# Optimization experiments

Measured on AMD Instinct MI355X. Metric: run time of the kernel, lower is better.

The kernel has to match this reference:

```python
import jax, jax.numpy as jnp
import numpy as np

L, D, H, HD, M = 4096, 1024, 16, 64, 4096
EPS = 1e-5


def setup_inputs() -> dict:
    key = jax.random.key(0)
    ks = jax.random.split(key, 12)
    hidden_states = jax.random.normal(ks[0], (L, D), dtype=jnp.float32)
    cu_seqlens = jnp.arange(5, dtype=jnp.int32) * (L // 4)  # [0,1024,2048,3072,4096]
    # rope freqs as cos/sin of random angles: (L, HD//2, 2)
    angles = jax.random.uniform(ks[1], (L, HD // 2), dtype=jnp.float32) * (2.0 * np.pi)
    rope_freqs = jnp.stack([jnp.cos(angles), jnp.sin(angles)], axis=-1)
    s = 0.02
    params = {
        "ln0_g": jnp.ones((D,), jnp.float32), "ln0_b": jnp.zeros((D,), jnp.float32),
        "ln1_g": jnp.ones((D,), jnp.float32), "ln1_b": jnp.zeros((D,), jnp.float32),
        "w_qkv": jax.random.normal(ks[2], (D, 3 * D), jnp.float32) * s,
        "w_o":   jax.random.normal(ks[3], (D, D), jnp.float32) * s,
        "w_fc0": jax.random.normal(ks[4], (D, M), jnp.float32) * s,
        "b_fc0": jnp.zeros((M,), jnp.float32),
        "w_fc1": jax.random.normal(ks[5], (M, D), jnp.float32) * s,
        "b_fc1": jnp.zeros((D,), jnp.float32),
    }
    return {"hidden_states": hidden_states, "cu_seqlens": cu_seqlens, "rope_freqs": rope_freqs, **params}


def _layernorm(x, g, b):
    mu = jnp.mean(x, axis=-1, keepdims=True)
    var = jnp.var(x, axis=-1, keepdims=True)
    return (x - mu) * jax.lax.rsqrt(var + EPS) * g + b


def _apply_rope(x, fc):
    # x: (L, H, HD); fc: (L, HD//2, 2) -> broadcast over heads
    xr = x.reshape(L, H, HD // 2, 2)
    a, b = xr[..., 0], xr[..., 1]
    c, s = fc[:, None, :, 0], fc[:, None, :, 1]
    out = jnp.stack([a * c - b * s, a * s + b * c], axis=-1)
    return out.reshape(L, H, HD)


def reference(hidden_states, cu_seqlens, rope_freqs, ln0_g, ln0_b, ln1_g, ln1_b,
              w_qkv, w_o, w_fc0, b_fc0, w_fc1, b_fc1):
    residual = hidden_states
    x = _layernorm(hidden_states, ln0_g, ln0_b)
    qkv = (x @ w_qkv).reshape(L, 3, H, HD)
    q, k, v = qkv[:, 0], qkv[:, 1], qkv[:, 2]
    q = _apply_rope(q, rope_freqs)
    k = _apply_rope(k, rope_freqs)
    # block-diagonal mask from cu_seqlens
    seg = jnp.searchsorted(cu_seqlens[1:], jnp.arange(L, dtype=cu_seqlens.dtype), side="right")
    mask = seg[:, None] == seg[None, :]  # (L, L)
    scale = 1.0 / np.sqrt(HD)
    scores = jnp.einsum("lhd,mhd->hlm", q, k) * scale
    scores = jnp.where(mask[None], scores, jnp.float32(-1e30))
    probs = jax.nn.softmax(scores, axis=-1)
    attn = jnp.einsum("hlm,mhd->lhd", probs, v).reshape(L, D)
    attn = attn @ w_o
    h = residual + attn
    y = _layernorm(h, ln1_g, ln1_b)
    y = jax.nn.gelu(y @ w_fc0 + b_fc0, approximate=False) @ w_fc1 + b_fc1
    return h + y
```

## Files before the change

### kernel.cpp

```cpp
#include <hip/hip_runtime.h>
#include <cstdint>
#include <cmath>

#define L_ 4096
#define D_ 1024
#define H_ 16
#define HD_ 64
#define M_ 4096

typedef __bf16 bf16_t;
typedef __attribute__((ext_vector_type(8))) __bf16 bf16x8;
typedef __attribute__((ext_vector_type(4))) __bf16 bf16x4;
typedef __attribute__((ext_vector_type(4))) float f32x4;

#define WAIT_VM0 0x0f70
#define WAIT_LGKM0 0xc07f

__device__ __forceinline__ f32x4 mfma16(bf16x8 a, bf16x8 b, f32x4 c) {
    return __builtin_amdgcn_mfma_f32_16x16x32_bf16(a, b, c, 0, 0, 0);
}

__device__ __forceinline__ void gload_lds16(const bf16_t* g, bf16_t* l) {
    __builtin_amdgcn_global_load_lds(
        (const __attribute__((address_space(1))) unsigned int*)(g),
        (__attribute__((address_space(3))) unsigned int*)(l), 16, 0, 0);
}

__device__ __forceinline__ float fast_exp2(float x) {
    float r;
    asm volatile("v_exp_f32 %0, %1" : "=v"(r) : "v"(x));
    return r;
}
__device__ __forceinline__ float fast_rcp(float x) {
    float r;
    asm volatile("v_rcp_f32 %0, %1" : "=v"(r) : "v"(x));
    return r;
}
__device__ __forceinline__ float gelu_f(float v) {
    float t = v * (0.7978845608f + 0.0356774081f * v * v);
    return v * fast_rcp(1.f + fast_exp2(-2.885390082f * t));
}

__global__ __launch_bounds__(256) void ln_kernel(const float* __restrict__ x,
                                                 const float* __restrict__ g,
                                                 const float* __restrict__ b,
                                                 bf16_t* __restrict__ out) {
    int row = blockIdx.x, tid = threadIdx.x;
    int wave = tid >> 6, lane = tid & 63;
    const f32x4* xr = (const f32x4*)(x + (long)row * D_);
    f32x4 v = xr[tid];
    float s = v.x + v.y + v.z + v.w;
    __shared__ float red[8];
#pragma unroll
    for (int off = 32; off > 0; off >>= 1) s += __shfl_down(s, off, 64);
    if (lane == 0) red[wave] = s;
    __syncthreads();
    float mean = (red[0] + red[1] + red[2] + red[3]) * (1.f / 1024.f);
    float s2 = 0.f;
#pragma unroll
    for (int i = 0; i < 4; i++) { float d = v[i] - mean; s2 += d * d; }
#pragma unroll
    for (int off = 32; off > 0; off >>= 1) s2 += __shfl_down(s2, off, 64);
    __syncthreads();
    if (lane == 0) red[wave] = s2;
    __syncthreads();
    float var = (red[0] + red[1] + red[2] + red[3]) * (1.f / 1024.f);
    float rstd = rsqrtf(var + 1e-5f);
    f32x4 g4 = ((const f32x4*)g)[tid];
    f32x4 b4 = ((const f32x4*)b)[tid];
    bf16x4 o;
#pragma unroll
    for (int i = 0; i < 4; i++) o[i] = (bf16_t)((v[i] - mean) * rstd * g4[i] + b4[i]);
    *(bf16x4*)(out + (long)row * D_ + tid * 4) = o;
}

__global__ __launch_bounds__(256) void transpose_all(
    const float* __restrict__ w_qkv, const float* __restrict__ w_o,
    const float* __restrict__ w_fc0, const float* __restrict__ w_fc1,
    bf16_t* __restrict__ t_qkv, bf16_t* __restrict__ t_o,
    bf16_t* __restrict__ t_fc0, bf16_t* __restrict__ t_fc1) {
    __shared__ float t[32][33];
    int bidx = blockIdx.x;
    const float* W;
    bf16_t* Wt;
    int K, N, tile;
    if (bidx < 3072) { W = w_qkv; Wt = t_qkv; K = 1024; N = 3072; tile = bidx; }
    else if (bidx < 4096) { W = w_o; Wt = t_o; K = 1024; N = 1024; tile = bidx - 3072; }
    else if (bidx < 8192) { W = w_fc0; Wt = t_fc0; K = 1024; N = 4096; tile = bidx - 4096; }
    else { W = w_fc1; Wt = t_fc1; K = 4096; N = 1024; tile = bidx - 8192; }
    int nt = N >> 5;
    int n0 = (tile % nt) * 32, k0 = (tile / nt) * 32;
    int tx = threadIdx.x & 31, ty = threadIdx.x >> 5;
#pragma unroll
    for (int r = 0; r < 32; r += 8)
        t[ty + r][tx] = W[(long)(k0 + ty + r) * N + n0 + tx];
    __syncthreads();
#pragma unroll
    for (int r = 0; r < 32; r += 8)
        Wt[(long)(n0 + ty + r) * K + k0 + tx] = (bf16_t)t[tx][ty + r];
}

__global__ __launch_bounds__(256) void vt_kernel(const bf16_t* __restrict__ qkv,
                                                 bf16_t* __restrict__ Vt) {
    __shared__ bf16_t t[32][33];
    int l0 = blockIdx.x * 32, c0 = blockIdx.y * 32;
    int tx = threadIdx.x & 31, ty = threadIdx.x >> 5;
#pragma unroll
    for (int r = 0; r < 32; r += 8)
        t[ty + r][tx] = qkv[(long)(l0 + ty + r) * 3072 + 2048 + c0 + tx];
    __syncthreads();
#pragma unroll
    for (int r = 0; r < 32; r += 8)
        Vt[(long)(c0 + ty + r) * 4096 + l0 + tx] = t[tx][ty + r];
}

__global__ __launch_bounds__(256) void rope_kernel(bf16_t* __restrict__ qkv,
                                                   const float* __restrict__ freqs) {
    const float k1 = 0.125f * 1.44269504089f;
    int idx = blockIdx.x * 256 + threadIdx.x;
    int g = idx & 7;
    int h = (idx >> 3) & 15;
    int l = idx >> 7;
    const float* f = freqs + (long)l * 64 + g * 8;
    f32x4 f0 = ((const f32x4*)f)[0];
    f32x4 f1 = ((const f32x4*)f)[1];
    float c[4] = {f0.x, f0.z, f1.x, f1.z};
    float s[4] = {f0.y, f0.w, f1.y, f1.w};
    bf16_t* qp = qkv + (long)l * 3072 + h * 64 + g * 8;
    bf16x8 q = *(bf16x8*)qp;
    bf16x8 k = *(bf16x8*)(qp + 1024);
    bf16x8 qo, ko;
#pragma unroll
    for (int e = 0; e < 4; e++) {
        float a = (float)q[2 * e], b = (float)q[2 * e + 1];
        qo[2 * e] = (bf16_t)((a * c[e] - b * s[e]) * k1);
        qo[2 * e + 1] = (bf16_t)((a * s[e] + b * c[e]) * k1);
        a = (float)k[2 * e]; b = (float)k[2 * e + 1];
        ko[2 * e] = (bf16_t)(a * c[e] - b * s[e]);
        ko[2 * e + 1] = (bf16_t)(a * s[e] + b * c[e]);
    }
    *(bf16x8*)qp = qo;
    *(bf16x8*)(qp + 1024) = ko;
}

#define STAGE_A(d, h, kt)                                                          \
    gload_lds16(aSt + (long)((h) * 128) * K + (kt), &SA[d][h][(wv * 16) * 64]);    \
    gload_lds16(aSt + (long)((h) * 128 + 8) * K + (kt), &SA[d][h][(wv * 16 + 8) * 64]);

#define STAGE_B(d, h, kt)                                                          \
    gload_lds16(bSt + (long)((h) * 128) * K + (kt), &SB[d][h][(wv * 16) * 64]);    \
    gload_lds16(bSt + (long)((h) * 128 + 8) * K + (kt), &SB[d][h][(wv * 16 + 8) * 64]);

#define RD_A(dst, src, rq)                                                          \
    _Pragma("unroll") for (int i_ = 0; i_ < 4; i_++) {                              \
        dst[i_][0] = *(const bf16x8*)&src[((rq) * 64 + i_ * 16 + l16) * 64 + sl0 * 8]; \
        dst[i_][1] = *(const bf16x8*)&src[((rq) * 64 + i_ * 16 + l16) * 64 + sl1 * 8]; \
    }

#define RD_B(dst, src, cq)                                                          \
    _Pragma("unroll") for (int j_ = 0; j_ < 2; j_++) {                              \
        dst[j_][0] = *(const bf16x8*)&src[(bro + (cq) * 32 + j_ * 16 + l16) * 64 + sl0 * 8]; \
        dst[j_][1] = *(const bf16x8*)&src[(bro + (cq) * 32 + j_ * 16 + l16) * 64 + sl1 * 8]; \
    }

#define MFMA_Q(rq, cq, Af, Bf)                                                      \
    _Pragma("unroll") for (int i_ = 0; i_ < 4; i_++)                                \
    _Pragma("unroll") for (int j_ = 0; j_ < 2; j_++) {                              \
        acc[(rq) * 4 + i_][(cq) * 2 + j_] =                                         \
            mfma16(Af[i_][0], Bf[j_][0], acc[(rq) * 4 + i_][(cq) * 2 + j_]);        \
        acc[(rq) * 4 + i_][(cq) * 2 + j_] =                                         \
            mfma16(Af[i_][1], Bf[j_][1], acc[(rq) * 4 + i_][(cq) * 2 + j_]);        \
    }

#define LGKM0() asm volatile("s_waitcnt lgkmcnt(0)" ::: "memory")
#define VMC(n) asm volatile("s_waitcnt vmcnt(" #n ")" ::: "memory")
#define BAR() __builtin_amdgcn_s_barrier()
#define PRIO1() __builtin_amdgcn_s_setprio(1)
#define PRIO0() __builtin_amdgcn_s_setprio(0)

template <int EPI>
__device__ __forceinline__ void gemm256_core(
    const bf16_t* __restrict__ A, const bf16_t* __restrict__ Bt,
    int K, int N, long bm, long bn, int kb, int ke,
    bf16_t* __restrict__ outB, const float* __restrict__ bias) {
    __shared__ __align__(16) bf16_t SA[2][2][128 * 64];
    __shared__ __align__(16) bf16_t SB[2][2][128 * 64];
    int tid = threadIdx.x;
    int wv = tid >> 6, lane = tid & 63;
    int quad = lane >> 4, l16 = lane & 15;
    int wm = wv >> 2, wn = wv & 3;
    int lr = lane >> 3;
    int sc = (lane & 7) ^ (lr & 7);
    int sl0 = quad ^ (l16 & 7);
    int sl1 = (4 + quad) ^ (l16 & 7);
    int bro = (wn & 1) * 64;

    const bf16_t* aSt = A + (bm + wv * 16 + lr) * (long)K + sc * 8;
    const bf16_t* bSt = Bt + (bn + wv * 16 + lr) * (long)K + sc * 8;
    const bf16_t* pa0 = SA[0][wm];
    const bf16_t* pa1 = SA[1][wm];
    const bf16_t* pb0 = SB[0][wn >> 1];
    const bf16_t* pb1 = SB[1][wn >> 1];

    f32x4 acc[8][4];
#pragma unroll
    for (int i = 0; i < 8; i++)
#pragma unroll
        for (int j = 0; j < 4; j++) acc[i][j] = (f32x4){0.f, 0.f, 0.f, 0.f};

    bf16x8 a0[4][2], a1[4][2], b0[2][2], b1[2][2];

    STAGE_B(0, 0, kb); STAGE_A(0, 0, kb); STAGE_B(0, 1, kb); STAGE_A(0, 1, kb);
    STAGE_B(1, 0, kb + 64); STAGE_A(1, 0, kb + 64); STAGE_B(1, 1, kb + 64);
    VMC(6);
    BAR();
    RD_A(a0, pa0, 0); RD_B(b0, pb0, 0);
    LGKM0();

    for (int k0 = kb; k0 < ke; k0 += 128) {
        int kt2 = (k0 + 128 < ke) ? k0 + 128 : kb;
        int kt3 = kt2 + 64;
        BAR(); STAGE_A(1, 1, k0 + 64);
        PRIO1(); MFMA_Q(0, 0, a0, b0); PRIO0();
        RD_B(b1, pb0, 1); LGKM0();
        BAR(); STAGE_B(0, 0, kt2);
        PRIO1(); MFMA_Q(0, 1, a0, b1); PRIO0();
        RD_A(a1, pa0, 1); LGKM0();
        BAR(); STAGE_A(0, 0, kt2);
        PRIO1(); MFMA_Q(1, 0, a1, b0); PRIO0();
        VMC(4);
        BAR(); STAGE_B(0, 1, kt2);
        PRIO1(); MFMA_Q(1, 1, a1, b1); PRIO0();
        RD_A(a0, pa1, 0); RD_B(b0, pb1, 0); LGKM0();
        BAR(); STAGE_A(0, 1, kt2);
        PRIO1(); MFMA_Q(0, 0, a0, b0); PRIO0();
        RD_B(b1, pb1, 1); LGKM0();
        BAR(); STAGE_B(1, 0, kt3);
        PRIO1(); MFMA_Q(0, 1, a0, b1); PRIO0();
        RD_A(a1, pa1, 1); LGKM0();
        BAR(); STAGE_A(1, 0, kt3);
        PRIO1(); MFMA_Q(1, 0, a1, b0); PRIO0();
        VMC(4);
        BAR(); STAGE_B(1, 1, kt3);
        PRIO1(); MFMA_Q(1, 1, a1, b1); PRIO0();
        RD_A(a0, pa0, 0); RD_B(b0, pb0, 0); LGKM0();
    }
    VMC(0);

#pragma unroll
    for (int ri = 0; ri < 8; ri++)
#pragma unroll
        for (int cj = 0; cj < 4; cj++)
#pragma unroll
            for (int r = 0; r < 4; r++) {
                long row = bm + wm * 128 + (ri >> 2) * 64 + (ri & 3) * 16 + quad * 4 + r;
                long col = bn + wn * 64 + (cj >> 1) * 32 + (cj & 1) * 16 + l16;
                long idx = row * (long)N + col;
                float v = acc[ri][cj][r];
                if (EPI == 0) {
                    outB[idx] = (bf16_t)v;
                } else {
                    v += bias[col];
                    outB[idx] = (bf16_t)gelu_f(v);
                }
            }
}

__global__ __launch_bounds__(512) void gemm256_qkv(const bf16_t* __restrict__ A,
                                                   const bf16_t* __restrict__ Bt,
                                                   bf16_t* __restrict__ outB) {
    int g = blockIdx.x & 7, w = blockIdx.x >> 3;
    int gm = g >> 2, gn = g & 3;
    long bm = (long)(gm * 8 + w / 3) * 256;
    long bn = (long)(gn * 3 + w % 3) * 256;
    gemm256_core<0>(A, Bt, 1024, 3072, bm, bn, 0, 1024, outB, nullptr);
}

__global__ __launch_bounds__(512) void gemm256_fc0(const bf16_t* __restrict__ A,
                                                   const bf16_t* __restrict__ Bt,
                                                   bf16_t* __restrict__ outB,
                                                   const float* __restrict__ bias) {
    int g = blockIdx.x & 7, w = blockIdx.x >> 3;
    int gm = g >> 2, gn = g & 3;
    long bm = (long)(gm * 8 + (w >> 2)) * 256;
    long bn = (long)(gn * 4 + (w & 3)) * 256;
    gemm256_core<2>(A, Bt, 1024, 4096, bm, bn, 0, 1024, outB, bias);
}

__global__ __launch_bounds__(512) void gemm256_fc1(const bf16_t* __restrict__ A,
                                                   const bf16_t* __restrict__ Bt,
                                                   bf16_t* __restrict__ P) {
    int g = blockIdx.x & 7, w = blockIdx.x >> 3;
    int z = g >> 1, gm = g & 1;
    long bm = (long)(gm * 8 + (w >> 2)) * 256;
    long bn = (long)(w & 3) * 256;
    gemm256_core<0>(A, Bt, 4096, 1024, bm, bn, z * 1024, z * 1024 + 1024,
                    P + (long)z * L_ * D_, nullptr);
}

__global__ __launch_bounds__(256) void reduce_fc1(const bf16_t* __restrict__ P,
                                                  const float* __restrict__ bias,
                                                  float* __restrict__ out) {
    long i = (long)blockIdx.x * 256 + threadIdx.x;
    f32x4 b = ((const f32x4*)bias)[i & 255];
    f32x4 v = ((f32x4*)out)[i];
#pragma unroll
    for (int z = 0; z < 4; z++) {
        bf16x4 p = ((const bf16x4*)(P + (long)z * L_ * D_))[i];
#pragma unroll
        for (int e = 0; e < 4; e++) v[e] += (float)p[e];
    }
    v.x += b.x; v.y += b.y; v.z += b.z; v.w += b.w;
    ((f32x4*)out)[i] = v;
}

__global__ __launch_bounds__(256) void gemm_bt64_res(const bf16_t* __restrict__ A,
                                                     const bf16_t* __restrict__ Bt,
                                                     int M, int N, int K,
                                                     float* __restrict__ outF,
                                                     const float* __restrict__ res) {
    __shared__ __align__(16) bf16_t As[128 * 64];
    __shared__ __align__(16) bf16_t Bs[64 * 64];
    int tid = threadIdx.x;
    int wave = tid >> 6, lane = tid & 63;
    int quad = lane >> 4, l16 = lane & 15;

    int g = blockIdx.x & 7, w = blockIdx.x >> 3;
    int bn_i = w & 15, bm_i = g * 4 + (w >> 4);
    long bm = (long)bm_i * 128, bn = (long)bn_i * 64;

    f32x4 acc[2][4];
#pragma unroll
    for (int i = 0; i < 2; i++)
#pragma unroll
        for (int j = 0; j < 4; j++) acc[i][j] = (f32x4){0.f, 0.f, 0.f, 0.f};

    int lr = lane >> 3;
    int sc = (lane & 7) ^ (lr & 7);
    const bf16_t* a_base = A + (bm + wave * 32 + lr) * (long)K + sc * 8;
    const bf16_t* b_base = Bt + (bn + wave * 16 + lr) * (long)K + sc * 8;

    for (int k0 = 0; k0 < K; k0 += 64) {
        __syncthreads();
#pragma unroll
        for (int i = 0; i < 4; i++)
            gload_lds16(a_base + k0 + (long)(8 * i) * K, &As[(wave * 32 + 8 * i) * 64]);
#pragma unroll
        for (int i = 0; i < 2; i++)
            gload_lds16(b_base + k0 + (long)(8 * i) * K, &Bs[(wave * 16 + 8 * i) * 64]);
        __builtin_amdgcn_s_waitcnt(WAIT_VM0);
        __syncthreads();

#pragma unroll
        for (int h = 0; h < 2; h++) {
            int sl = (h * 4 + quad) ^ (l16 & 7);
            bf16x8 af[2], bfr[4];
#pragma unroll
            for (int i = 0; i < 2; i++)
                af[i] = *(const bf16x8*)&As[(wave * 32 + i * 16 + l16) * 64 + sl * 8];
#pragma unroll
            for (int j = 0; j < 4; j++)
                bfr[j] = *(const bf16x8*)&Bs[(j * 16 + l16) * 64 + sl * 8];
#pragma unroll
            for (int i = 0; i < 2; i++)
#pragma unroll
                for (int j = 0; j < 4; j++)
                    acc[i][j] = mfma16(af[i], bfr[j], acc[i][j]);
        }
    }

#pragma unroll
    for (int i = 0; i < 2; i++)
#pragma unroll
        for (int j = 0; j < 4; j++)
#pragma unroll
            for (int r = 0; r < 4; r++) {
                long row = bm + wave * 32 + i * 16 + quad * 4 + r;
                long col = bn + j * 16 + l16;
                long idx = row * (long)N + col;
                outF[idx] = acc[i][j][r] + res[idx];
            }
}

__global__ __launch_bounds__(256) void attn_kernel(const bf16_t* __restrict__ qkv,
                                                   const bf16_t* __restrict__ Vt,
                                                   const int* __restrict__ cu,
                                                   bf16_t* __restrict__ out) {
    __shared__ __align__(16) bf16_t QPs[4 * 16 * 72];
    __shared__ __align__(16) bf16_t Ks[2][64 * 64];
    __shared__ __align__(16) bf16_t Vs[2][64 * 64];

    int tid = threadIdx.x, wave = tid >> 6, lane = tid & 63;
    int quad = lane >> 4, l16 = lane & 15;

    int g = blockIdx.x & 7, w = blockIdx.x >> 3;
    int head = (w & 1) * 8 + g;
    int qt = (w >> 1) & 15;
    int seg = w >> 5;
    int s0 = cu[seg], s1 = cu[seg + 1];
    int r0 = s0 + qt * 64;
    const long hoff = (long)head * 64;

    bf16_t* Qs = QPs;
    bf16_t* Psw = &QPs[wave * 16 * 72];

    int lr = lane >> 3;
    int sc = (lane & 7) ^ (lr & 7);
    int sl0 = (0 * 4 + quad) ^ (l16 & 7);
    int sl1 = (1 * 4 + quad) ^ (l16 & 7);

#pragma unroll
    for (int i = 0; i < 2; i++) {
        int row = wave * 16 + i * 8 + lr;
        gload_lds16(qkv + (long)(r0 + row) * 3072 + hoff + sc * 8,
                    &Qs[(wave * 16 + i * 8) * 64]);
    }
    __builtin_amdgcn_s_waitcnt(WAIT_VM0);
    __syncthreads();
    bf16x8 aq0 = *(const bf16x8*)&Qs[(wave * 16 + l16) * 64 + sl0 * 8];
    bf16x8 aq1 = *(const bf16x8*)&Qs[(wave * 16 + l16) * 64 + sl1 * 8];

    bf16x8 ones;
#pragma unroll
    for (int e = 0; e < 8; e++) ones[e] = (bf16_t)1.0f;

    f32x4 o[4];
#pragma unroll
    for (int j = 0; j < 4; j++) o[j] = (f32x4){0.f, 0.f, 0.f, 0.f};
    f32x4 lacc = (f32x4){0.f, 0.f, 0.f, 0.f};

    for (int kt = s0; kt < s1; kt += 128) {
        __syncthreads();
#pragma unroll
        for (int i = 0; i < 2; i++) {
            int row = wave * 16 + i * 8 + lr;
            long kr0 = (long)(kt + row) * 3072 + 1024 + hoff + sc * 8;
            gload_lds16(qkv + kr0, &Ks[0][(wave * 16 + i * 8) * 64]);
            gload_lds16(qkv + kr0 + (long)64 * 3072, &Ks[1][(wave * 16 + i * 8) * 64]);
            long vr0 = (hoff + row) * (long)4096 + kt + sc * 8;
            gload_lds16(Vt + vr0, &Vs[0][(wave * 16 + i * 8) * 64]);
            gload_lds16(Vt + vr0 + 64, &Vs[1][(wave * 16 + i * 8) * 64]);
        }
        __builtin_amdgcn_s_waitcnt(WAIT_VM0);
        __syncthreads();

#pragma unroll
        for (int half = 0; half < 2; half++) {
            f32x4 sacc[4];
#pragma unroll
            for (int j = 0; j < 4; j++) sacc[j] = (f32x4){0.f, 0.f, 0.f, 0.f};
#pragma unroll
            for (int j = 0; j < 4; j++) {
                bf16x8 b0 = *(const bf16x8*)&Ks[half][(j * 16 + l16) * 64 + sl0 * 8];
                bf16x8 b1 = *(const bf16x8*)&Ks[half][(j * 16 + l16) * 64 + sl1 * 8];
                sacc[j] = mfma16(aq0, b0, sacc[j]);
                sacc[j] = mfma16(aq1, b1, sacc[j]);
            }

#pragma unroll
            for (int j = 0; j < 4; j++)
#pragma unroll
                for (int r = 0; r < 4; r++)
                    Psw[(quad * 4 + r) * 72 + j * 16 + l16] = (bf16_t)fast_exp2(sacc[j][r]);

            __builtin_amdgcn_s_waitcnt(WAIT_LGKM0);

            bf16x8 ap0 = *(const bf16x8*)&Psw[l16 * 72 + 0 * 32 + quad * 8];
            bf16x8 ap1 = *(const bf16x8*)&Psw[l16 * 72 + 1 * 32 + quad * 8];
#pragma unroll
            for (int j2 = 0; j2 < 4; j2++) {
                bf16x8 b0 = *(const bf16x8*)&Vs[half][(j2 * 16 + l16) * 64 + sl0 * 8];
                bf16x8 b1 = *(const bf16x8*)&Vs[half][(j2 * 16 + l16) * 64 + sl1 * 8];
                o[j2] = mfma16(ap0, b0, o[j2]);
                o[j2] = mfma16(ap1, b1, o[j2]);
            }
            lacc = mfma16(ap0, ones, lacc);
            lacc = mfma16(ap1, ones, lacc);
        }
    }

#pragma unroll
    for (int r = 0; r < 4; r++) {
        float inv = fast_rcp(lacc[r]);
        int row = r0 + wave * 16 + quad * 4 + r;
#pragma unroll
        for (int j2 = 0; j2 < 4; j2++)
            out[(long)row * 1024 + head * 64 + j2 * 16 + l16] = (bf16_t)(o[j2][r] * inv);
    }
}

extern "C" void kernel_launch(void* const* d_in, const int* in_sizes, int n_in,
                              void* d_out, int out_size, void* d_ws, size_t ws_size,
                              hipStream_t stream) {
    const float* hidden = (const float*)d_in[0];
    const int* cu = (const int*)d_in[1];
    const float* freqs = (const float*)d_in[2];
    const float* ln0_g = (const float*)d_in[3];
    const float* ln0_b = (const float*)d_in[4];
    const float* ln1_g = (const float*)d_in[5];
    const float* ln1_b = (const float*)d_in[6];
    const float* w_qkv = (const float*)d_in[7];
    const float* w_o = (const float*)d_in[8];
    const float* w_fc0 = (const float*)d_in[9];
    const float* b_fc0 = (const float*)d_in[10];
    const float* w_fc1 = (const float*)d_in[11];
    const float* b_fc1 = (const float*)d_in[12];
    float* out = (float*)d_out;

    char* ws = (char*)d_ws;
    bf16_t* qkv = (bf16_t*)(ws);
    bf16_t* attn = (bf16_t*)(ws + ((size_t)24 << 20));
    bf16_t* act = (bf16_t*)(ws);
    bf16_t* x_bf = (bf16_t*)(ws + ((size_t)32 << 20));
    bf16_t* Vt = x_bf;
    bf16_t* y_bf = x_bf;
    bf16_t* fc1p = (bf16_t*)(ws + ((size_t)40 << 20));
    bf16_t* wqkvT = (bf16_t*)(ws + ((size_t)72 << 20));
    bf16_t* woT = (bf16_t*)(ws + ((size_t)78 << 20));
    bf16_t* wfc0T = (bf16_t*)(ws + ((size_t)80 << 20));
    bf16_t* wfc1T = (bf16_t*)(ws + ((size_t)88 << 20));
    float* h = out;

    transpose_all<<<12288, 256, 0, stream>>>(w_qkv, w_o, w_fc0, w_fc1,
                                             wqkvT, woT, wfc0T, wfc1T);

    ln_kernel<<<L_, 256, 0, stream>>>(hidden, ln0_g, ln0_b, x_bf);

    gemm256_qkv<<<192, 512, 0, stream>>>(x_bf, wqkvT, qkv);

    rope_kernel<<<(L_ * H_ * 8) / 256, 256, 0, stream>>>(qkv, freqs);
    vt_kernel<<<dim3(4096 / 32, 1024 / 32), 256, 0, stream>>>(qkv, Vt);

    attn_kernel<<<1024, 256, 0, stream>>>(qkv, Vt, cu, attn);

    gemm_bt64_res<<<512, 256, 0, stream>>>(
        attn, woT, L_, 1024, 1024, h, hidden);

    ln_kernel<<<L_, 256, 0, stream>>>(h, ln1_g, ln1_b, y_bf);

    gemm256_fc0<<<256, 512, 0, stream>>>(y_bf, wfc0T, act, b_fc0);

    gemm256_fc1<<<256, 512, 0, stream>>>(act, wfc1T, fc1p);
    reduce_fc1<<<(L_ * D_ / 4) / 256, 256, 0, stream>>>(fc1p, b_fc1, out);
}
```

Baseline: 314.2 us.

## Coarsen GEMM main-loop schedule into four phases with paired stage loads

Restructures the software-pipelined bf16 GEMM main loop from eight barrier-separated phases into four. Each phase now issues both halves of the A or B tile load together and runs two MFMA quadrants back to back. The prologue now prefetches both k-stages completely, including the A half that was previously loaded inside the loop, and waits with VMC(8). The goal is to halve the number of workgroup barriers and LDS wait points per iteration. In exchange, memory issue and compute are interleaved more coarsely, and more loads are in flight at each wait.

```diff
diff --git a/kernel.cpp b/kernel.cpp
--- a/kernel.cpp
+++ b/kernel.cpp
@@ -210,40 +210,31 @@
 
     bf16x8 a0[4][2], a1[4][2], b0[2][2], b1[2][2];
 
-    STAGE_B(0, 0, kb); STAGE_A(0, 0, kb); STAGE_B(0, 1, kb); STAGE_A(0, 1, kb);
-    STAGE_B(1, 0, kb + 64); STAGE_A(1, 0, kb + 64); STAGE_B(1, 1, kb + 64);
-    VMC(6);
+    STAGE_B(0, 0, kb); STAGE_B(0, 1, kb); STAGE_A(0, 0, kb); STAGE_A(0, 1, kb);
+    STAGE_B(1, 0, kb + 64); STAGE_B(1, 1, kb + 64);
+    STAGE_A(1, 0, kb + 64); STAGE_A(1, 1, kb + 64);
+    VMC(8);
     BAR();
-    RD_A(a0, pa0, 0); RD_B(b0, pb0, 0);
+    RD_A(a0, pa0, 0); RD_B(b0, pb0, 0); RD_B(b1, pb0, 1);
     LGKM0();
 
     for (int k0 = kb; k0 < ke; k0 += 128) {
         int kt2 = (k0 + 128 < ke) ? k0 + 128 : kb;
         int kt3 = kt2 + 64;
-        BAR(); STAGE_A(1, 1, k0 + 64);
-        PRIO1(); MFMA_Q(0, 0, a0, b0); PRIO0();
-        RD_B(b1, pb0, 1); LGKM0();
-        BAR(); STAGE_B(0, 0, kt2);
-        PRIO1(); MFMA_Q(0, 1, a0, b1); PRIO0();
+        BAR(); STAGE_B(0, 0, kt2); STAGE_B(0, 1, kt2);
+        PRIO1(); MFMA_Q(0, 0, a0, b0); MFMA_Q(0, 1, a0, b1); PRIO0();
         RD_A(a1, pa0, 1); LGKM0();
-        BAR(); STAGE_A(0, 0, kt2);
-        PRIO1(); MFMA_Q(1, 0, a1, b0); PRIO0();
         VMC(4);
-        BAR(); STAGE_B(0, 1, kt2);
-        PRIO1(); MFMA_Q(1, 1, a1, b1); PRIO0();
-        RD_A(a0, pa1, 0); RD_B(b0, pb1, 0); LGKM0();
-        BAR(); STAGE_A(0, 1, kt2);
-        PRIO1(); MFMA_Q(0, 0, a0, b0); PRIO0();
-        RD_B(b1, pb1, 1); LGKM0();
-        BAR(); STAGE_B(1, 0, kt3);
-        PRIO1(); MFMA_Q(0, 1, a0, b1); PRIO0();
+        BAR(); STAGE_A(0, 0, kt2); STAGE_A(0, 1, kt2);
+        PRIO1(); MFMA_Q(1, 0, a1, b0); MFMA_Q(1, 1, a1, b1); PRIO0();
+        RD_A(a0, pa1, 0); RD_B(b0, pb1, 0); RD_B(b1, pb1, 1); LGKM0();
+        BAR(); STAGE_B(1, 0, kt3); STAGE_B(1, 1, kt3);
+        PRIO1(); MFMA_Q(0, 0, a0, b0); MFMA_Q(0, 1, a0, b1); PRIO0();
         RD_A(a1, pa1, 1); LGKM0();
-        BAR(); STAGE_A(1, 0, kt3);
-        PRIO1(); MFMA_Q(1, 0, a1, b0); PRIO0();
         VMC(4);
-        BAR(); STAGE_B(1, 1, kt3);
-        PRIO1(); MFMA_Q(1, 1, a1, b1); PRIO0();
-        RD_A(a0, pa0, 0); RD_B(b0, pb0, 0); LGKM0();
+        BAR(); STAGE_A(1, 0, kt3); STAGE_A(1, 1, kt3);
+        PRIO1(); MFMA_Q(1, 0, a1, b0); MFMA_Q(1, 1, a1, b1); PRIO0();
+        RD_A(a0, pa0, 0); RD_B(b0, pb0, 0); RD_B(b1, pb0, 1); LGKM0();
     }
     VMC(0);
 
```

Measured after the change: 311.2 us. No clear change (-0.9%).
